# Performance work log

Hardware: AMD Instinct MI355X
Metric: run time of the kernel (lower is better)

## Reference

```python
import jax, jax.numpy as jnp
import numpy as np

DIM = 1024
B = 8192
DT_REF_BASE = 1.0


def _cayley(raw_re, raw_im):
    # A = skew-Hermitian-ish combo per original code
    A = (raw_re - raw_re.T) * 0.5 + 1j * ((raw_im + raw_im.T) * 0.5)
    I = jnp.eye(A.shape[0], dtype=A.dtype)
    return jnp.linalg.solve(I - A, I + A)


def setup_inputs() -> dict:
    key = jax.random.key(0)
    ks = jax.random.split(key, 16)
    d = DIM
    g = d // 2  # n_groups = 2, equal group sizes
    return {
        "h_prev": jax.random.normal(ks[0], (B, d), jnp.float32),
        "x_input": jax.random.normal(ks[1], (B, d), jnp.float32),
        "dt": jax.random.uniform(ks[2], (B,), jnp.float32),
        "u_raw_re": jax.random.normal(ks[3], (d, d), jnp.float32) * 0.01,
        "u_raw_im": jax.random.normal(ks[4], (d, d), jnp.float32) * 0.01,
        "v_raw_re": jax.random.normal(ks[5], (d, d), jnp.float32) * 0.01,
        "v_raw_im": jax.random.normal(ks[6], (d, d), jnp.float32) * 0.01,
        "log_sigma": jnp.zeros((d,), jnp.float32),
        "ld": jax.random.normal(ks[7], (d,), jnp.float32) * 0.5 - 2.0,
        "lf": jnp.concatenate([
            2.0 * jax.random.normal(ks[8], (g,), jnp.float32),
            0.1 * jax.random.normal(ks[9], (g,), jnp.float32),
        ]),
        "dt_scaler": jnp.concatenate([0.1 * jnp.ones((g,), jnp.float32),
                                      10.0 * jnp.ones((g,), jnp.float32)]),
        "src_re": jax.random.normal(ks[10], (d,), jnp.float32) * 0.01,
        "src_im": jax.random.normal(ks[11], (d,), jnp.float32) * 0.01,
        "law_re": jax.random.normal(ks[12], (d,), jnp.float32) * 0.01,
        "law_im": jax.random.normal(ks[13], (d,), jnp.float32) * 0.01,
        "sel_w": jax.random.normal(ks[14], (2 * d, 2 * d), jnp.float32) * 0.01,
        "sel_b": jax.random.normal(ks[15], (2 * d,), jnp.float32) * 0.01,
    }


def reference(h_prev, x_input, dt, u_raw_re, u_raw_im, v_raw_re, v_raw_im,
              log_sigma, ld, lf, dt_scaler, src_re, src_im, law_re, law_im,
              sel_w, sel_b):
    # --- Cayley basis (shared between encode/decode) ---
    U = _cayley(u_raw_re, u_raw_im)                       # [D, D] complex
    V = _cayley(v_raw_re, v_raw_im)
    s = jnp.exp(log_sigma).astype(U.dtype)
    s_inv = jnp.exp(-log_sigma).astype(U.dtype)
    M_inv = (V * s_inv[None, :]) @ U.conj().T             # V @ diag(1/s) @ U^H
    M = (U * s[None, :]) @ V.conj().T                     # U @ diag(s) @ V^H

    encode = lambda x: x.astype(M_inv.dtype) @ M_inv.T
    h_tilde = encode(h_prev)[:, None, :]                  # [B, 1, D]
    x_tilde = encode(x_input)[:, None, :]                 # [B, 1, D]
    x_state = x_tilde[:, 0, :]                            # [B, D]

    # --- selective Lambda ---
    lam_static = (-jnp.exp(ld) + 1j * lf) + (law_re + 1j * law_im)  # [D]
    x_cat = jnp.concatenate([x_state.real, x_state.imag], axis=-1)  # [B, 2D]
    delta = x_cat @ sel_w.T + sel_b                                  # [B, 2D]
    d_re, d_im = jnp.split(delta, 2, axis=-1)
    Lam = lam_static[None, :] + (d_re + 1j * d_im)                   # [B, D]

    # --- transition operators ---
    dt_ref_eff = DT_REF_BASE * dt_scaler                  # [D]
    dt_n = dt[:, None] / dt_ref_eff                       # [B, D]
    Z = Lam * dt_n.astype(Lam.dtype)
    mask = jnp.abs(Z) < 1e-4
    safe_Z = jnp.where(mask, jnp.ones_like(Z), Z)
    phi1 = jnp.where(mask, 1.0 + 0.5 * Z + Z * Z / 6.0,
                     (jnp.exp(Z) - 1.0) / safe_Z)
    op_decay = jnp.exp(Z)                                 # [B, D]
    op_forcing = phi1 * (dt_n * dt_ref_eff).astype(Z.dtype)

    bias = src_re + 1j * src_im                           # [D]
    h_next = h_tilde * op_decay[:, None, :] + (x_tilde + bias) * op_forcing[:, None, :]
    # eval mode / noise term omitted (deterministic reference)
    return h_next @ M.T                                   # [B, 1, D] complex64
```

## Files before the change

### kernel.cpp

```cpp
#include <hip/hip_runtime.h>
#include <hip/hip_bf16.h>

#define Dd 1024
#define Bb 8192

typedef unsigned short u16;
typedef __attribute__((ext_vector_type(8))) short short8;
typedef __attribute__((ext_vector_type(4))) float f32x4;
typedef __attribute__((ext_vector_type(4))) float float4v;

static constexpr size_t DD  = (size_t)Dd * Dd;
static constexpr size_t BD  = (size_t)Bb * Dd;
static constexpr size_t MBy = 1ull << 20;

__device__ __forceinline__ float bf2f(u16 v) {
  union { unsigned u; float f; } c; c.u = ((unsigned)v) << 16; return c.f;
}
__device__ __forceinline__ u16 f2bf(float f) {
  union { float f; unsigned u; } c; c.f = f;
  return (u16)((c.u + 0x7fffu + ((c.u >> 16) & 1u)) >> 16);
}

union U64 { u16 u[4]; unsigned long long v; };

struct ZP { const u16* Ah; const u16* Al; const u16* Bh; const u16* Bl; void* C; void* C2; float alpha; float beta; };
struct GArgs { ZP z[8]; int K, lda, ldb; long ldc; int cstride; };

template<int OUT>
__device__ __forceinline__ void c_store(const ZP& p, long cidx, float acc) {
  float v = acc * p.alpha;
  if constexpr (OUT == 1) {
    ((u16*)p.C)[cidx] = f2bf(v);
  } else if constexpr (OUT == 2) {
    u16 h = f2bf(v);
    ((u16*)p.C)[cidx] = h;
    ((u16*)p.C2)[cidx] = f2bf(v - bf2f(h));
  } else {
    float* C = (float*)p.C;
    if (p.beta != 0.0f) v += p.beta * C[cidx];
    C[cidx] = v;
  }
}

template<int MODE, int OUT>
__global__ __launch_bounds__(256) void gemm_nt(GArgs a) {
  constexpr bool X2 = (MODE != 0);
  constexpr int BK  = X2 ? 32 : 64;
  constexpr int BUFS = 16384;
  __shared__ __align__(16) u16 smem[2 * BUFS];
  const ZP p = a.z[blockIdx.z];
  const int tid  = threadIdx.x;
  const int lane = tid & 63, wv = tid >> 6;

  int bx = blockIdx.x, by = blockIdx.y;
  {
    const int gx = gridDim.x;
    const int nwg = gx * gridDim.y;
    if ((nwg & 7) == 0 && nwg >= 16) {
      const int flat = by * gx + bx;
      const int ch = nwg >> 3;
      const int nf = (flat & 7) * ch + (flat >> 3);
      bx = nf % gx; by = nf / gx;
    }
  }

  const long brow = (long)by * 128, bcol = (long)bx * 128;
  const int wm = (wv & 1) * 64, wn = (wv >> 1) * 64;
  const int srow = wv * 8 + (lane >> 3);
  const int sgc64 = ((lane & 7) ^ (lane >> 3)) * 8;
  const int sgc32 = ((tid & 3) ^ ((tid >> 3) & 3)) * 8;

  f32x4 acc[4][4];
#pragma unroll
  for (int i = 0; i < 4; ++i)
#pragma unroll
    for (int j = 0; j < 4; ++j) { f32x4 zv = {0.f, 0.f, 0.f, 0.f}; acc[i][j] = zv; }

  auto STAGE = [&](int kt, int buf) {
    u16* base = smem + buf * BUFS;
    if constexpr (!X2) {
      u16* As = base;
      u16* Bs = base + 8192;
#pragma unroll
      for (int i = 0; i < 4; ++i) {
        const int rr = i * 32 + srow;
        const int lb = (i * 32 + wv * 8) * 64;
        const u16* ga = p.Ah + (brow + rr) * (long)a.lda + kt + sgc64;
        const u16* gb = p.Bh + (bcol + rr) * (long)a.ldb + kt + sgc64;
        __builtin_amdgcn_global_load_lds((const __attribute__((address_space(1))) void*)ga,
                                         (__attribute__((address_space(3))) void*)(As + lb), 16, 0, 0);
        __builtin_amdgcn_global_load_lds((const __attribute__((address_space(1))) void*)gb,
                                         (__attribute__((address_space(3))) void*)(Bs + lb), 16, 0, 0);
      }
    } else {
#pragma unroll
      for (int pass = 0; pass < 2; ++pass) {
        const int row = pass * 64 + (tid >> 2);
        const int lb = pass * 2048 + tid * 8;
        const u16* ga = p.Ah + (brow + row) * (long)a.lda + kt + sgc32;
        const u16* gb = p.Bh + (bcol + row) * (long)a.ldb + kt + sgc32;
        const u16* ga2 = p.Al + (brow + row) * (long)a.lda + kt + sgc32;
        const u16* gb2 = p.Bl + (bcol + row) * (long)a.ldb + kt + sgc32;
        __builtin_amdgcn_global_load_lds((const __attribute__((address_space(1))) void*)ga,
                                         (__attribute__((address_space(3))) void*)(base + lb), 16, 0, 0);
        __builtin_amdgcn_global_load_lds((const __attribute__((address_space(1))) void*)gb,
                                         (__attribute__((address_space(3))) void*)(base + 4096 + lb), 16, 0, 0);
        __builtin_amdgcn_global_load_lds((const __attribute__((address_space(1))) void*)ga2,
                                         (__attribute__((address_space(3))) void*)(base + 8192 + lb), 16, 0, 0);
        __builtin_amdgcn_global_load_lds((const __attribute__((address_space(1))) void*)gb2,
                                         (__attribute__((address_space(3))) void*)(base + 12288 + lb), 16, 0, 0);
      }
    }
  };

  auto COMPUTE = [&](int buf) {
    u16* base = smem + buf * BUFS;
    if constexpr (!X2) {
      u16* As = base;
      u16* Bs = base + 8192;
#pragma unroll
      for (int kk = 0; kk < 64; kk += 32) {
        const int jf = (kk >> 3) + (lane >> 4);
        const int cs = ((jf ^ (lane & 7)) << 3);
        short8 af[4], bfv[4];
#pragma unroll
        for (int i = 0; i < 4; ++i) {
          af[i]  = *(const short8*)(As + (wm + i * 16 + (lane & 15)) * 64 + cs);
          bfv[i] = *(const short8*)(Bs + (wn + i * 16 + (lane & 15)) * 64 + cs);
        }
#pragma unroll
        for (int i = 0; i < 4; ++i)
#pragma unroll
          for (int j = 0; j < 4; ++j)
            acc[i][j] = __builtin_amdgcn_mfma_f32_16x16x32_bf16(af[i], bfv[j], acc[i][j], 0, 0, 0);
      }
    } else {
      const int jf = lane >> 4;
      const int cs = ((jf ^ ((lane >> 1) & 3)) << 3);
      short8 af[4], bfv[4], al[4], bl[4];
#pragma unroll
      for (int i = 0; i < 4; ++i) {
        const int ra = (wm + i * 16 + (lane & 15)) * 32 + cs;
        const int rb = (wn + i * 16 + (lane & 15)) * 32 + cs;
        af[i]  = *(const short8*)(base + ra);
        bfv[i] = *(const short8*)(base + 4096 + rb);
        al[i]  = *(const short8*)(base + 8192 + ra);
        bl[i]  = *(const short8*)(base + 12288 + rb);
      }
#pragma unroll
      for (int i = 0; i < 4; ++i)
#pragma unroll
        for (int j = 0; j < 4; ++j) {
          acc[i][j] = __builtin_amdgcn_mfma_f32_16x16x32_bf16(af[i], bfv[j], acc[i][j], 0, 0, 0);
          acc[i][j] = __builtin_amdgcn_mfma_f32_16x16x32_bf16(al[i], bfv[j], acc[i][j], 0, 0, 0);
          acc[i][j] = __builtin_amdgcn_mfma_f32_16x16x32_bf16(af[i], bl[j], acc[i][j], 0, 0, 0);
        }
    }
  };

  const int nkt = a.K / BK;
  STAGE(0, 0);
  __syncthreads();
  int cur = 0;
  for (int t = 0; t < nkt - 1; ++t) {
    STAGE((t + 1) * BK, cur ^ 1);
    COMPUTE(cur);
    __syncthreads();
    cur ^= 1;
  }
  COMPUTE(cur);

  const long crow = brow + wm + ((lane >> 4) * 4);
  const long ccol = bcol + wn + (lane & 15);
#pragma unroll
  for (int i = 0; i < 4; ++i)
#pragma unroll
    for (int j = 0; j < 4; ++j)
#pragma unroll
      for (int r = 0; r < 4; ++r) {
        const long cidx = (crow + i * 16 + r) * a.ldc + (ccol + j * 16) * (long)a.cstride;
        c_store<OUT>(p, cidx, acc[i][j][r]);
      }
}

template<int OUT>
__global__ __launch_bounds__(512, 1) void gemm_nt256(GArgs a) {
  constexpr int BUFS = 32768;
  __shared__ __align__(16) u16 smem[2 * BUFS];
  const ZP p = a.z[blockIdx.z];
  const int tid  = threadIdx.x;
  const int lane = tid & 63, wv = tid >> 6;
  const int wr = wv >> 2, wc = wv & 3;

  int bx = blockIdx.x, by = blockIdx.y;
  {
    const int gx = gridDim.x;
    const int nwg = gx * gridDim.y;
    if ((nwg & 7) == 0 && nwg >= 16) {
      const int flat = by * gx + bx;
      const int ch = nwg >> 3;
      const int nf = (flat & 7) * ch + (flat >> 3);
      bx = nf % gx; by = nf / gx;
    }
  }

  const long brow = (long)by * 256, bcol = (long)bx * 256;
  const int sgc = ((tid & 7) ^ ((tid >> 3) & 7)) * 8;

  f32x4 acc[8][4];
#pragma unroll
  for (int i = 0; i < 8; ++i)
#pragma unroll
    for (int j = 0; j < 4; ++j) { f32x4 zv = {0.f, 0.f, 0.f, 0.f}; acc[i][j] = zv; }

  auto STAGE = [&](int kt, int buf) {
    u16* As = smem + buf * BUFS;
    u16* Bs = As + 16384;
#pragma unroll
    for (int i = 0; i < 4; ++i) {
      const int rr = i * 64 + (tid >> 3);
      const int lb = i * 4096 + tid * 8;
      const u16* ga = p.Ah + (brow + rr) * (long)a.lda + kt + sgc;
      const u16* gb = p.Bh + (bcol + rr) * (long)a.ldb + kt + sgc;
      __builtin_amdgcn_global_load_lds((const __attribute__((address_space(1))) void*)ga,
                                       (__attribute__((address_space(3))) void*)(As + lb), 16, 0, 0);
      __builtin_amdgcn_global_load_lds((const __attribute__((address_space(1))) void*)gb,
                                       (__attribute__((address_space(3))) void*)(Bs + lb), 16, 0, 0);
    }
  };

  auto COMPUTE = [&](int buf) {
    u16* As = smem + buf * BUFS;
    u16* Bs = As + 16384;
#pragma unroll
    for (int kk = 0; kk < 64; kk += 32) {
      const int jf = (kk >> 3) + (lane >> 4);
      const int cs = ((jf ^ (lane & 7)) << 3);
      short8 af[8], bfv[4];
#pragma unroll
      for (int i = 0; i < 8; ++i)
        af[i] = *(const short8*)(As + (wr * 128 + i * 16 + (lane & 15)) * 64 + cs);
#pragma unroll
      for (int j = 0; j < 4; ++j)
        bfv[j] = *(const short8*)(Bs + (wc * 64 + j * 16 + (lane & 15)) * 64 + cs);
#pragma unroll
      for (int i = 0; i < 8; ++i)
#pragma unroll
        for (int j = 0; j < 4; ++j)
          acc[i][j] = __builtin_amdgcn_mfma_f32_16x16x32_bf16(af[i], bfv[j], acc[i][j], 0, 0, 0);
    }
  };

  const int nkt = a.K >> 6;
  STAGE(0, 0);
  __syncthreads();
  int cur = 0;
  for (int t = 0; t < nkt - 1; ++t) {
    STAGE((t + 1) * 64, cur ^ 1);
    COMPUTE(cur);
    __syncthreads();
    cur ^= 1;
  }
  COMPUTE(cur);

  const long crow = brow + wr * 128 + ((lane >> 4) * 4);
  const long ccol = bcol + wc * 64 + (lane & 15);
#pragma unroll
  for (int i = 0; i < 8; ++i)
#pragma unroll
    for (int j = 0; j < 4; ++j)
#pragma unroll
      for (int r = 0; r < 4; ++r) {
        const long cidx = (crow + i * 16 + r) * a.ldc + (ccol + j * 16) * (long)a.cstride;
        c_store<OUT>(p, cidx, acc[i][j][r]);
      }
}

#define TLOAD(ldsbuf, srcp) do { \
  _Pragma("unroll") \
  for (int i_ = 0; i_ < 4; ++i_) { \
    int row_ = ty + i_ * 16; \
    float4v v_ = *(const float4v*)((srcp) + (size_t)row_ * Dd + tx * 4); \
    ldsbuf[row_][tx * 4 + 0] = v_[0]; ldsbuf[row_][tx * 4 + 1] = v_[1]; \
    ldsbuf[row_][tx * 4 + 2] = v_[2]; ldsbuf[row_][tx * 4 + 3] = v_[3]; \
  } } while (0)

__global__ void k_buildA(const float* ur, const float* ui, const float* vr, const float* vi,
                         float* Af32, u16* Ahi, u16* Alo, u16* AsumH, u16* AsumL) {
  __shared__ float ldsA[64][65], ldsB[64][65];
  const int y = blockIdx.z;
  const int tx = threadIdx.x & 15, ty = threadIdx.x >> 4;
  const int R0 = blockIdx.y * 64, C0 = blockIdx.x * 64;
  const float* re = y ? vr : ur; const float* im = y ? vi : ui;
  TLOAD(ldsA, re + (size_t)C0 * Dd + R0);
  TLOAD(ldsB, im + (size_t)C0 * Dd + R0);
  __syncthreads();
#pragma unroll
  for (int i = 0; i < 4; ++i) {
    const int r = R0 + ty + i * 16;
    const size_t base = (size_t)r * Dd + C0 + tx * 4;
    float4v vre = *(const float4v*)(re + base);
    float4v vim = *(const float4v*)(im + base);
    float4v oar, oai;
    U64 ph, pl, pih, pil, sh, sl;
#pragma unroll
    for (int j = 0; j < 4; ++j) {
      float are = 0.5f * (vre[j] - ldsA[tx * 4 + j][ty + i * 16]);
      float aim = 0.5f * (vim[j] + ldsB[tx * 4 + j][ty + i * 16]);
      oar[j] = are; oai[j] = aim;
      u16 h = f2bf(are); ph.u[j] = h; pl.u[j] = f2bf(are - bf2f(h));
      h = f2bf(aim); pih.u[j] = h; pil.u[j] = f2bf(aim - bf2f(h));
      float s = are + aim; h = f2bf(s); sh.u[j] = h; sl.u[j] = f2bf(s - bf2f(h));
    }
    const size_t pr = (size_t)y * 2 * DD + base, pi = pr + DD;
    *(float4v*)(Af32 + pr) = oar; *(float4v*)(Af32 + pi) = oai;
    *(unsigned long long*)(Ahi + pr) = ph.v; *(unsigned long long*)(Alo + pr) = pl.v;
    *(unsigned long long*)(Ahi + pi) = pih.v; *(unsigned long long*)(Alo + pi) = pil.v;
    const size_t ps = (size_t)y * DD + base;
    *(unsigned long long*)(AsumH + ps) = sh.v; *(unsigned long long*)(AsumL + ps) = sl.v;
  }
}

__global__ void k_sq(const float* T, float* A2u, float* A2v, u16* A2T, u16* A2Tsum) {
  __shared__ float ldsA[64][65], ldsB[64][65];
  const int y = blockIdx.z;
  const int tx = threadIdx.x & 15, ty = threadIdx.x >> 4;
  const int R0 = blockIdx.y * 64, C0 = blockIdx.x * 64;
  const float* t0p = T + (size_t)y * 3 * DD;
  const float* t2p = t0p + 2 * DD;
  TLOAD(ldsA, t2p + (size_t)C0 * Dd + R0);
  __syncthreads();
  float* A2 = y ? A2v : A2u;
  float xr[4][4], xi[4][4];
#pragma unroll
  for (int i = 0; i < 4; ++i) {
    const size_t base = (size_t)(R0 + ty + i * 16) * Dd + C0 + tx * 4;
    float4v v0 = *(const float4v*)(t0p + base);
    float4v v1 = *(const float4v*)(t0p + DD + base);
    float4v v2 = *(const float4v*)(t2p + base);
    float4v oar, oai;
#pragma unroll
    for (int j = 0; j < 4; ++j) {
      float a2re = -v0[j] - v1[j];
      float a2im = v2[j] - ldsA[tx * 4 + j][ty + i * 16];
      xr[i][j] = a2re; xi[i][j] = a2im;
      oar[j] = a2re; oai[j] = a2im;
    }
    *(float4v*)(A2 + base) = oar;
    *(float4v*)(A2 + DD + base) = oai;
  }
  __syncthreads();
#pragma unroll
  for (int i = 0; i < 4; ++i)
#pragma unroll
    for (int j = 0; j < 4; ++j) {
      ldsA[ty + i * 16][tx * 4 + j] = xr[i][j];
      ldsB[ty + i * 16][tx * 4 + j] = xi[i][j];
    }
  __syncthreads();
#pragma unroll
  for (int i = 0; i < 4; ++i) {
    const int cc = C0 + ty + i * 16;
    const size_t tb = (size_t)cc * Dd + R0 + tx * 4;
    U64 ph, pih, sh;
#pragma unroll
    for (int j = 0; j < 4; ++j) {
      float a2re = ldsA[tx * 4 + j][ty + i * 16];
      float a2im = ldsB[tx * 4 + j][ty + i * 16];
      ph.u[j] = f2bf(a2re); pih.u[j] = f2bf(a2im);
      sh.u[j] = f2bf(a2re + a2im);
    }
    const size_t qr = (size_t)y * 2 * DD + tb;
    *(unsigned long long*)(A2T + qr) = ph.v;
    *(unsigned long long*)(A2T + qr + DD) = pih.v;
    *(unsigned long long*)(A2Tsum + (size_t)y * DD + tb) = sh.v;
  }
}

__global__ void k_x0n(const float* Af32, const float* A2u, const float* A2v, const float* T,
                      float* Xf32, u16* Xhi, u16* XThi, u16* XsumH, u16* XTsumH) {
  __shared__ float ldsA[64][65], ldsB[64][65];
  const int y = blockIdx.z;
  const int tx = threadIdx.x & 15, ty = threadIdx.x >> 4;
  const int R0 = blockIdx.y * 64, C0 = blockIdx.x * 64;
  const float* t0p = T + (size_t)y * 3 * DD;
  const float* A2 = y ? A2v : A2u;
  float xr[4][4], xi[4][4];
#pragma unroll
  for (int i = 0; i < 4; ++i) {
    const int r = R0 + ty + i * 16;
    const size_t base = (size_t)r * Dd + C0 + tx * 4;
    float4v v0 = *(const float4v*)(t0p + base);
    float4v v1 = *(const float4v*)(t0p + DD + base);
    float4v v2 = *(const float4v*)(t0p + 2 * DD + base);
    const size_t pr = (size_t)y * 2 * DD + base, pi = pr + DD;
    float4v ar = *(const float4v*)(Af32 + pr);
    float4v ai = *(const float4v*)(Af32 + pi);
    float4v a2r = *(const float4v*)(A2 + base);
    float4v a2i = *(const float4v*)(A2 + DD + base);
    float4v oxr, oxi;
    U64 ph, pih, sh;
#pragma unroll
    for (int j = 0; j < 4; ++j) {
      const int c = C0 + tx * 4 + j;
      float xre = ar[j] + a2r[j] + (v0[j] - v1[j]) + (r == c ? 1.0f : 0.0f);
      float xim = ai[j] + a2i[j] + (v2[j] - v0[j] - v1[j]);
      xr[i][j] = xre; xi[i][j] = xim;
      oxr[j] = xre; oxi[j] = xim;
      ph.u[j] = f2bf(xre); pih.u[j] = f2bf(xim);
      sh.u[j] = f2bf(xre + xim);
    }
    *(float4v*)(Xf32 + pr) = oxr; *(float4v*)(Xf32 + pi) = oxi;
    *(unsigned long long*)(Xhi + pr) = ph.v; *(unsigned long long*)(Xhi + pi) = pih.v;
    *(unsigned long long*)(XsumH + (size_t)y * DD + base) = sh.v;
  }
  __syncthreads();
#pragma unroll
  for (int i = 0; i < 4; ++i)
#pragma unroll
    for (int j = 0; j < 4; ++j) {
      ldsA[ty + i * 16][tx * 4 + j] = xr[i][j];
      ldsB[ty + i * 16][tx * 4 + j] = xi[i][j];
    }
  __syncthreads();
#pragma unroll
  for (int i = 0; i < 4; ++i) {
    const int cc = C0 + ty + i * 16;
    const size_t tb = (size_t)cc * Dd + R0 + tx * 4;
    U64 ph, pih, sh;
#pragma unroll
    for (int j = 0; j < 4; ++j) {
      float xre = ldsA[tx * 4 + j][ty + i * 16];
      float xim = ldsB[tx * 4 + j][ty + i * 16];
      ph.u[j] = f2bf(xre); pih.u[j] = f2bf(xim);
      sh.u[j] = f2bf(xre + xim);
    }
    const size_t qr = (size_t)y * 2 * DD + tb;
    *(unsigned long long*)(XThi + qr) = ph.v;
    *(unsigned long long*)(XThi + qr + DD) = pih.v;
    *(unsigned long long*)(XTsumH + (size_t)y * DD + tb) = sh.v;
  }
}

__global__ void k_wt(const float* Xf32, const float* T, u16* WThi, u16* WTsumH, float idc) {
  __shared__ float lds[64][65];
  const int y = blockIdx.z;
  const int tx = threadIdx.x & 15, ty = threadIdx.x >> 4;
  const int N0 = blockIdx.y * 64, K0 = blockIdx.x * 64;
  const float* t1p = T + (size_t)y * 3 * DD;
  const float* xrp = Xf32 + (size_t)y * 2 * DD;
  float wre[4][4], wim[4][4];
#pragma unroll
  for (int i = 0; i < 4; ++i)
#pragma unroll
    for (int j = 0; j < 4; ++j) {
      wre[i][j] = ((N0 + ty + i * 16) == (K0 + tx * 4 + j)) ? idc : 0.0f;
      wim[i][j] = 0.0f;
    }
  const float* planes[5] = {t1p, t1p + DD, t1p + 2 * DD, xrp, xrp + DD};
#pragma unroll
  for (int p = 0; p < 5; ++p) {
    TLOAD(lds, planes[p] + (size_t)K0 * Dd + N0);
    __syncthreads();
#pragma unroll
    for (int i = 0; i < 4; ++i)
#pragma unroll
      for (int j = 0; j < 4; ++j) {
        float v = lds[tx * 4 + j][ty + i * 16];
        if (p == 0) { wre[i][j] += v; wim[i][j] -= v; }
        else if (p == 1) { wre[i][j] -= v; wim[i][j] -= v; }
        else if (p == 2) { wim[i][j] += v; }
        else if (p == 3) { wre[i][j] -= v; }
        else { wim[i][j] -= v; }
      }
    __syncthreads();
  }
#pragma unroll
  for (int i = 0; i < 4; ++i) {
    const size_t base = (size_t)(N0 + ty + i * 16) * Dd + K0 + tx * 4;
    U64 ph, pih, sh;
#pragma unroll
    for (int j = 0; j < 4; ++j) {
      ph.u[j] = f2bf(wre[i][j]); pih.u[j] = f2bf(wim[i][j]);
      sh.u[j] = f2bf(wre[i][j] + wim[i][j]);
    }
    const size_t pr = (size_t)y * 2 * DD + base;
    *(unsigned long long*)(WThi + pr) = ph.v;
    *(unsigned long long*)(WThi + pr + DD) = pih.v;
    *(unsigned long long*)(WTsumH + (size_t)y * DD + base) = sh.v;
  }
}

__global__ void k_xn(const float* T, float* Xf32, u16* Xhi, u16* XThi, u16* XsumH, u16* XTsumH,
                     u16* Xlo, u16* XTlo, u16* XTsumL) {
  __shared__ float ldsA[64][65], ldsB[64][65];
  const int y = blockIdx.z;
  const int tx = threadIdx.x & 15, ty = threadIdx.x >> 4;
  const int R0 = blockIdx.y * 64, C0 = blockIdx.x * 64;
  const float* t1p = T + (size_t)y * 3 * DD;
  float xr[4][4], xi[4][4];
#pragma unroll
  for (int i = 0; i < 4; ++i) {
    const size_t base = (size_t)(R0 + ty + i * 16) * Dd + C0 + tx * 4;
    float4v v1 = *(const float4v*)(t1p + base);
    float4v v2 = *(const float4v*)(t1p + DD + base);
    float4v v3 = *(const float4v*)(t1p + 2 * DD + base);
    float4v oxr, oxi;
    U64 ph, pih, sh, plr, pli;
#pragma unroll
    for (int j = 0; j < 4; ++j) {
      float xre = v1[j] - v2[j];
      float xim = v3[j] - v1[j] - v2[j];
      xr[i][j] = xre; xi[i][j] = xim;
      oxr[j] = xre; oxi[j] = xim;
      u16 hr = f2bf(xre), hi_ = f2bf(xim);
      ph.u[j] = hr; pih.u[j] = hi_;
      sh.u[j] = f2bf(xre + xim);
      plr.u[j] = f2bf(xre - bf2f(hr)); pli.u[j] = f2bf(xim - bf2f(hi_));
    }
    const size_t pr = (size_t)y * 2 * DD + base, pi = pr + DD;
    *(float4v*)(Xf32 + pr) = oxr; *(float4v*)(Xf32 + pi) = oxi;
    *(unsigned long long*)(Xhi + pr) = ph.v; *(unsigned long long*)(Xhi + pi) = pih.v;
    *(unsigned long long*)(XsumH + (size_t)y * DD + base) = sh.v;
    if (Xlo) {
      *(unsigned long long*)(Xlo + pr) = plr.v;
      *(unsigned long long*)(Xlo + pi) = pli.v;
    }
  }
  __syncthreads();
#pragma unroll
  for (int i = 0; i < 4; ++i)
#pragma unroll
    for (int j = 0; j < 4; ++j) {
      ldsA[ty + i * 16][tx * 4 + j] = xr[i][j];
      ldsB[ty + i * 16][tx * 4 + j] = xi[i][j];
    }
  __syncthreads();
#pragma unroll
  for (int i = 0; i < 4; ++i) {
    const int cc = C0 + ty + i * 16;
    const size_t tb = (size_t)cc * Dd + R0 + tx * 4;
    U64 ph, pih, sh, plr, pli, sl;
#pragma unroll
    for (int j = 0; j < 4; ++j) {
      float xre = ldsA[tx * 4 + j][ty + i * 16];
      float xim = ldsB[tx * 4 + j][ty + i * 16];
      u16 hr = f2bf(xre), hi_ = f2bf(xim);
      ph.u[j] = hr; pih.u[j] = hi_;
      float s = xre + xim; u16 hs = f2bf(s);
      sh.u[j] = hs;
      plr.u[j] = f2bf(xre - bf2f(hr)); pli.u[j] = f2bf(xim - bf2f(hi_));
      sl.u[j] = f2bf(s - bf2f(hs));
    }
    const size_t qr = (size_t)y * 2 * DD + tb;
    *(unsigned long long*)(XThi + qr) = ph.v;
    *(unsigned long long*)(XThi + qr + DD) = pih.v;
    *(unsigned long long*)(XTsumH + (size_t)y * DD + tb) = sh.v;
    if (Xlo) {
      *(unsigned long long*)(XTlo + qr) = plr.v;
      *(unsigned long long*)(XTlo + qr + DD) = pli.v;
      *(unsigned long long*)(XTsumL + (size_t)y * DD + tb) = sl.v;
    }
  }
}

__global__ void k_finalUV(const float* Xf32, const float* T, const float* logsig,
                          u16* VsHi, u16* VsLo, u16* UHi, u16* ULo, u16* UsHi, u16* VHi,
                          u16* UdifH, u16* UdifL, u16* UssumH, u16* VssumH, u16* VssumL, u16* VdifH) {
  const int y = blockIdx.y;
  const size_t idx = (size_t)blockIdx.x * 256 + threadIdx.x;
  const size_t r = idx >> 10, c = idx & 1023;
  const size_t t0 = (size_t)y * 3 * DD;
  float t1 = T[t0 + idx], t2 = T[t0 + DD + idx], t3 = T[t0 + 2 * DD + idx];
  const size_t pr = (size_t)y * 2 * DD + idx, pi = pr + DD;
  float cre = 2.0f * (Xf32[pr] + (t1 - t2)) - (r == c ? 1.0f : 0.0f);
  float cim = 2.0f * (Xf32[pi] + (t3 - t1 - t2));
  if (y == 0) {
    u16 h = f2bf(cre); UHi[idx] = h; ULo[idx] = f2bf(cre - bf2f(h));
    h = f2bf(cim); UHi[DD + idx] = h; ULo[DD + idx] = f2bf(cim - bf2f(h));
    float d = cre - cim; h = f2bf(d); UdifH[idx] = h; UdifL[idx] = f2bf(d - bf2f(h));
    float s = expf(logsig[c]);
    UsHi[idx] = f2bf(cre * s); UsHi[DD + idx] = f2bf(cim * s);
    UssumH[idx] = f2bf((cre + cim) * s);
  } else {
    VHi[idx] = f2bf(cre); VHi[DD + idx] = f2bf(cim);
    VdifH[idx] = f2bf(cre - cim);
    float si = expf(-logsig[c]);
    float a = cre * si, b = cim * si;
    u16 h = f2bf(a); VsHi[idx] = h; VsLo[idx] = f2bf(a - bf2f(h));
    h = f2bf(b); VsHi[DD + idx] = h; VsLo[DD + idx] = f2bf(b - bf2f(h));
    float ss = (cre + cim) * si; h = f2bf(ss); VssumH[idx] = h; VssumL[idx] = f2bf(ss - bf2f(h));
  }
}

__global__ void k_cmb_M(const float* T, u16* MiRe, u16* MiIm, u16* MiTcH, u16* MiTcL,
                        u16* Mcat) {
  __shared__ float ldsA[64][65], ldsB[64][65];
  const int tx = threadIdx.x & 15, ty = threadIdx.x >> 4;
  const int R0 = blockIdx.y * 64, C0 = blockIdx.x * 64;
#pragma unroll
  for (int i = 0; i < 4; ++i) {
    const size_t base = (size_t)(R0 + ty + i * 16) * Dd + C0 + tx * 4;
    const size_t r = R0 + ty + i * 16;
    float4v g1 = *(const float4v*)(T + base);
    float4v g2 = *(const float4v*)(T + DD + base);
    float4v g3 = *(const float4v*)(T + 2 * DD + base);
    float4v h1 = *(const float4v*)(T + 3 * DD + base);
    float4v h2 = *(const float4v*)(T + 4 * DD + base);
    float4v h3 = *(const float4v*)(T + 5 * DD + base);
    U64 pir, pii, pmr, pmi;
#pragma unroll
    for (int j = 0; j < 4; ++j) {
      float mire = g1[j] + g2[j];
      float miim = g3[j] - g1[j] + g2[j];
      float mre  = h1[j] + h2[j];
      float mim  = h3[j] - h1[j] + h2[j];
      pir.u[j] = f2bf(mire); pii.u[j] = f2bf(miim);
      pmr.u[j] = f2bf(mre);  pmi.u[j] = f2bf(mim);
      ldsA[ty + i * 16][tx * 4 + j] = mire;
      ldsB[ty + i * 16][tx * 4 + j] = miim;
    }
    *(unsigned long long*)(MiRe + base) = pir.v;
    *(unsigned long long*)(MiIm + base) = pii.v;
    const size_t mb = r * 2048 + C0 + tx * 4;
    *(unsigned long long*)(Mcat + mb) = pmr.v;
    *(unsigned long long*)(Mcat + mb + 1024) = pmi.v;
  }
  __syncthreads();
#pragma unroll
  for (int i = 0; i < 4; ++i) {
    const int cc = C0 + ty + i * 16;
    const size_t o = (size_t)cc * 2048 + R0 + tx * 4;
    U64 rh, rl, ih, il;
#pragma unroll
    for (int j = 0; j < 4; ++j) {
      float mire = ldsA[tx * 4 + j][ty + i * 16];
      float miim = ldsB[tx * 4 + j][ty + i * 16];
      u16 h = f2bf(mire); rh.u[j] = h; rl.u[j] = f2bf(mire - bf2f(h));
      h = f2bf(miim); ih.u[j] = h; il.u[j] = f2bf(miim - bf2f(h));
    }
    *(unsigned long long*)(MiTcH + o) = rh.v;
    *(unsigned long long*)(MiTcL + o) = rl.v;
    *(unsigned long long*)(MiTcH + o + 1024) = ih.v;
    *(unsigned long long*)(MiTcL + o + 1024) = il.v;
  }
}

__global__ void k_split4(const float* src, u16* hi, u16* lo) {
  const size_t i4 = (size_t)blockIdx.x * 256 + threadIdx.x;
  float4v v = ((const float4v*)src)[i4];
  U64 oh, ol;
#pragma unroll
  for (int j = 0; j < 4; ++j) {
    u16 h = f2bf(v[j]);
    oh.u[j] = h; ol.u[j] = f2bf(v[j] - bf2f(h));
  }
  ((unsigned long long*)hi)[i4] = oh.v;
  ((unsigned long long*)lo)[i4] = ol.v;
}

__global__ void k_splitB(const float* x, const float* hsrc, u16* xh, u16* xl, u16* hb) {
  const size_t i4 = (size_t)blockIdx.x * 256 + threadIdx.x;
  float4v xv = ((const float4v*)x)[i4];
  float4v hv = ((const float4v*)hsrc)[i4];
  U64 oh, ol, ob;
#pragma unroll
  for (int j = 0; j < 4; ++j) {
    u16 h = f2bf(xv[j]);
    oh.u[j] = h;
    ol.u[j] = f2bf(xv[j] - bf2f(h));
    ob.u[j] = f2bf(hv[j]);
  }
  ((unsigned long long*)xh)[i4] = oh.v;
  ((unsigned long long*)xl)[i4] = ol.v;
  ((unsigned long long*)hb)[i4] = ob.v;
}

__global__ void k_pointwise(const u16* HtCat, const u16* XtCat,
                            const float* delta, const float* dt, const float* ld, const float* lf,
                            const float* dts, const float* sre, const float* sim,
                            const float* lwre, const float* lwim, const float* selb,
                            u16* Hncat, float imSign) {
  const int b = blockIdx.x;
  const int c0 = threadIdx.x * 4;
  const size_t ro = (size_t)b * 2048 + c0;
  const float dtv = dt[b];
  float4v dre4 = *(const float4v*)(delta + ro);
  float4v dim4 = *(const float4v*)(delta + ro + 1024);
  float4v sbR = *(const float4v*)(selb + c0);
  float4v sbI = *(const float4v*)(selb + 1024 + c0);
  float4v ld4 = *(const float4v*)(ld + c0);
  float4v lf4 = *(const float4v*)(lf + c0);
  float4v dts4 = *(const float4v*)(dts + c0);
  float4v sre4 = *(const float4v*)(sre + c0);
  float4v sim4 = *(const float4v*)(sim + c0);
  float4v lwr4 = *(const float4v*)(lwre + c0);
  float4v lwi4 = *(const float4v*)(lwim + c0);
  U64 htR, htI, xtR, xtI;
  htR.v = *(const unsigned long long*)(HtCat + ro);
  htI.v = *(const unsigned long long*)(HtCat + ro + 1024);
  xtR.v = *(const unsigned long long*)(XtCat + ro);
  xtI.v = *(const unsigned long long*)(XtCat + ro + 1024);
  U64 oR, oI;
#pragma unroll
  for (int j = 0; j < 4; ++j) {
    float lamre = -expf(ld4[j]) + lwr4[j] + dre4[j] + sbR[j];
    float lamim = lf4[j] + lwi4[j] + dim4[j] + sbI[j];
    float dtn = dtv / dts4[j];
    float zre = lamre * dtn, zim = lamim * dtn;
    float r2 = zre * zre + zim * zim;
    float er = expf(zre); float sn, cs; __sincosf(zim, &sn, &cs);
    float dcre = er * cs, dcim = er * sn;
    float p1re, p1im;
    if (r2 < 1e-8f) {
      p1re = 1.0f + 0.5f * zre + (zre * zre - zim * zim) * (1.0f / 6.0f);
      p1im = 0.5f * zim + (zre * zim) * (1.0f / 3.0f);
    } else {
      float inv = 1.0f / r2;
      float nre = dcre - 1.0f, nim = dcim;
      p1re = (nre * zre + nim * zim) * inv;
      p1im = (nim * zre - nre * zim) * inv;
    }
    float fre = p1re * dtv, fim = p1im * dtv;
    float hre = bf2f(htR.u[j]), him = bf2f(htI.u[j]);
    float xre = bf2f(xtR.u[j]) + sre4[j], xim = bf2f(xtI.u[j]) + sim4[j];
    float ore = hre * dcre - him * dcim + xre * fre - xim * fim;
    float oim = hre * dcim + him * dcre + xre * fim + xim * fre;
    oR.u[j] = f2bf(ore); oI.u[j] = f2bf(imSign * oim);
  }
  *(unsigned long long*)(Hncat + ro) = oR.v;
  *(unsigned long long*)(Hncat + ro + 1024) = oI.v;
}

__global__ void k_fill(float* p, size_t n, float v) {
  const size_t idx = (size_t)blockIdx.x * 256 + threadIdx.x;
  if (idx < n) p[idx] = v;
}

static void launch_gemm(int mode, int out, int M, int N, int K, int lda, int ldb,
                        long ldc, int cstride, int nz, const ZP* z, hipStream_t s) {
  GArgs a; a.K = K; a.lda = lda; a.ldb = ldb; a.ldc = ldc; a.cstride = cstride;
  for (int i = 0; i < 8; ++i) a.z[i] = z[i < nz ? i : 0];
  dim3 g(N / 128, M / 128, nz), blk(256);
  if (mode == 1 && out == 0)      gemm_nt<1, 0><<<g, blk, 0, s>>>(a);
  else if (mode == 1 && out == 2) gemm_nt<1, 2><<<g, blk, 0, s>>>(a);
  else if (out == 1)              gemm_nt<0, 1><<<g, blk, 0, s>>>(a);
  else                            gemm_nt<0, 0><<<g, blk, 0, s>>>(a);
}

static void launch_gemm256(int out, int M, int N, int K, int lda, int ldb,
                           long ldc, int cstride, int nz, const ZP* z, hipStream_t s) {
  GArgs a; a.K = K; a.lda = lda; a.ldb = ldb; a.ldc = ldc; a.cstride = cstride;
  for (int i = 0; i < 8; ++i) a.z[i] = z[i < nz ? i : 0];
  dim3 g(N / 256, M / 256, nz), blk(512);
  if (out == 1) gemm_nt256<1><<<g, blk, 0, s>>>(a);
  else          gemm_nt256<0><<<g, blk, 0, s>>>(a);
}

extern "C" void kernel_launch(void* const* d_in, const int* in_sizes, int n_in,
                              void* d_out, int out_size, void* d_ws, size_t ws_size,
                              hipStream_t stream) {
  const float* h_prev  = (const float*)d_in[0];
  const float* x_input = (const float*)d_in[1];
  const float* dt      = (const float*)d_in[2];
  const float* ur      = (const float*)d_in[3];
  const float* ui      = (const float*)d_in[4];
  const float* vr      = (const float*)d_in[5];
  const float* vi      = (const float*)d_in[6];
  const float* logsig  = (const float*)d_in[7];
  const float* ld      = (const float*)d_in[8];
  const float* lf      = (const float*)d_in[9];
  const float* dts     = (const float*)d_in[10];
  const float* sre     = (const float*)d_in[11];
  const float* sim     = (const float*)d_in[12];
  const float* lwre    = (const float*)d_in[13];
  const float* lwim    = (const float*)d_in[14];
  const float* sel_w   = (const float*)d_in[15];
  const float* sel_b   = (const float*)d_in[16];
  float* out = (float*)d_out;
  char* ws = (char*)d_ws;

  const bool realOnly = ((size_t)out_size == BD);
  const bool interleaved = ((size_t)out_size == 2 * BD);
  if ((!realOnly && !interleaved) || ws_size < 224 * MBy) {
    k_fill<<<dim3(((size_t)out_size + 255) / 256), dim3(256), 0, stream>>>(out, (size_t)out_size, 1e9f);
    return;
  }

  u16* MiRe_b = (u16*)(ws + 0 * MBy);
  u16* MiIm_b = (u16*)(ws + 2 * MBy);
  u16* Mcat   = (u16*)(ws + 4 * MBy);
  u16* G_hi   = (u16*)(ws + 8 * MBy);
  u16* G_lo   = (u16*)(ws + 12 * MBy);
  char* AR = ws + 16 * MBy;
  float* Af32   = (float*)(AR + 0);
  u16* Ahi      = (u16*)(AR + 16 * MBy);
  u16* Alo      = (u16*)(AR + 24 * MBy);
  u16* AsumH    = (u16*)(AR + 32 * MBy);
  u16* AsumL    = (u16*)(AR + 36 * MBy);
  float* Xf32   = (float*)(AR + 40 * MBy);
  u16* Xhi      = (u16*)(AR + 56 * MBy);
  u16* Xlo      = (u16*)(AR + 64 * MBy);
  u16* XThi     = (u16*)(AR + 72 * MBy);
  u16* XTlo     = (u16*)(AR + 80 * MBy);
  u16* XsumH    = (u16*)(AR + 88 * MBy);
  u16* XTsumH   = (u16*)(AR + 92 * MBy);
  u16* XTsumL   = (u16*)(AR + 96 * MBy);
  u16* WThi     = (u16*)(AR + 100 * MBy);
  u16* WTsumH   = (u16*)(AR + 108 * MBy);
  float* T      = (float*)(AR + 112 * MBy);
  u16* VsHi     = (u16*)(AR + 136 * MBy);
  u16* VsLo     = (u16*)(AR + 140 * MBy);
  u16* UHi      = (u16*)(AR + 144 * MBy);
  u16* ULo      = (u16*)(AR + 148 * MBy);
  u16* UsHi     = (u16*)(AR + 152 * MBy);
  u16* VHi      = (u16*)(AR + 156 * MBy);
  u16* UdifH    = (u16*)(AR + 160 * MBy);
  u16* UdifL    = (u16*)(AR + 162 * MBy);
  u16* UssumH   = (u16*)(AR + 164 * MBy);
  u16* VssumH   = (u16*)(AR + 166 * MBy);
  u16* VssumL   = (u16*)(AR + 168 * MBy);
  u16* VdifH    = (u16*)(AR + 170 * MBy);
  u16* MiTcH    = (u16*)(AR + 172 * MBy);
  u16* MiTcL    = (u16*)(AR + 176 * MBy);
  u16* W_hi     = (u16*)(AR + 180 * MBy);
  u16* W_lo     = (u16*)(AR + 188 * MBy);
  float* A2u    = (float*)(AR + 64 * MBy);
  float* A2v    = (float*)(AR + 80 * MBy);
  u16* A2T      = (u16*)(AR + 100 * MBy);
  u16* A2Tsum   = (u16*)(AR + 108 * MBy);
  u16* Hb     = (u16*)(AR + 0);
  u16* XbHi   = (u16*)(AR + 16 * MBy);
  u16* XbLo   = (u16*)(AR + 32 * MBy);
  u16* HtCat  = (u16*)(AR + 48 * MBy);
  u16* XtCat  = (u16*)(AR + 80 * MBy);
  float* delta= (float*)(AR + 112 * MBy);
  u16* Hncat  = (u16*)(AR + 176 * MBy);

  dim3 b256(256);
  const dim3 tdd(16, 16, 2);

  k_buildA<<<tdd, b256, 0, stream>>>(ur, ui, vr, vi, Af32, Ahi, Alo, AsumH, AsumL);

  {
    ZP z[6];
    for (int y = 0; y < 2; ++y) {
      const u16* are = Ahi + (size_t)y * 2 * DD; const u16* aim = are + DD;
      float* t = T + (size_t)y * 3 * DD;
      z[y*3+0] = {are, nullptr, are, nullptr, t,          nullptr, 1.f, 0.f};
      z[y*3+1] = {aim, nullptr, aim, nullptr, t + DD,     nullptr, 1.f, 0.f};
      z[y*3+2] = {are, nullptr, aim, nullptr, t + 2*DD,   nullptr, 1.f, 0.f};
    }
    launch_gemm(0, 0, 1024, 1024, 1024, 1024, 1024, 1024, 1, 6, z, stream);
  }
  k_sq<<<tdd, b256, 0, stream>>>(T, A2u, A2v, A2T, A2Tsum);
  {
    ZP z[6];
    for (int y = 0; y < 2; ++y) {
      const u16* are = Ahi + (size_t)y*2*DD; const u16* aim = are + DD;
      const u16* a2r = A2T + (size_t)y*2*DD; const u16* a2i = a2r + DD;
      float* t = T + (size_t)y*3*DD;
      z[y*3+0] = {are, nullptr, a2r, nullptr, t,        nullptr, 1.f, 0.f};
      z[y*3+1] = {aim, nullptr, a2i, nullptr, t + DD,   nullptr, 1.f, 0.f};
      z[y*3+2] = {AsumH + (size_t)y*DD, nullptr, A2Tsum + (size_t)y*DD, nullptr, t + 2*DD, nullptr, 1.f, 0.f};
    }
    launch_gemm(0, 0, 1024, 1024, 1024, 1024, 1024, 1024, 1, 6, z, stream);
  }
  k_x0n<<<tdd, b256, 0, stream>>>(Af32, A2u, A2v, T, Xf32, Xhi, XThi, XsumH, XTsumH);

  {
    ZP z[6];
    for (int y = 0; y < 2; ++y) {
      const u16* are = Ahi + (size_t)y*2*DD; const u16* aim = are + DD;
      const u16* xtr = XThi + (size_t)y*2*DD; const u16* xti = xtr + DD;
      float* t = T + (size_t)y*3*DD;
      z[y*3+0] = {are, nullptr, xtr, nullptr, t,        nullptr, 1.f, 0.f};
      z[y*3+1] = {aim, nullptr, xti, nullptr, t + DD,   nullptr, 1.f, 0.f};
      z[y*3+2] = {AsumH + (size_t)y*DD, nullptr, XTsumH + (size_t)y*DD, nullptr, t + 2*DD, nullptr, 1.f, 0.f};
    }
    launch_gemm(0, 0, 1024, 1024, 1024, 1024, 1024, 1024, 1, 6, z, stream);
  }
  k_wt<<<tdd, b256, 0, stream>>>(Xf32, T, WThi, WTsumH, 2.0f);
  {
    ZP z[6];
    for (int y = 0; y < 2; ++y) {
      const u16* xre = Xhi + (size_t)y*2*DD; const u16* xim = xre + DD;
      const u16* wtr = WThi + (size_t)y*2*DD; const u16* wti = wtr + DD;
      float* t = T + (size_t)y*3*DD;
      z[y*3+0] = {xre, nullptr, wtr, nullptr, t,        nullptr, 1.f, 0.f};
      z[y*3+1] = {xim, nullptr, wti, nullptr, t + DD,   nullptr, 1.f, 0.f};
      z[y*3+2] = {XsumH + (size_t)y*DD, nullptr, WTsumH + (size_t)y*DD, nullptr, t + 2*DD, nullptr, 1.f, 0.f};
    }
    launch_gemm(0, 0, 1024, 1024, 1024, 1024, 1024, 1024, 1, 6, z, stream);
  }
  k_xn<<<tdd, b256, 0, stream>>>(T, Xf32, Xhi, XThi, XsumH, XTsumH, Xlo, XTlo, XTsumL);

  {
    ZP z[6];
    for (int y = 0; y < 2; ++y) {
      const u16* areh = Ahi + (size_t)y*2*DD; const u16* aimh = areh + DD;
      const u16* arel = Alo + (size_t)y*2*DD; const u16* aiml = arel + DD;
      const u16* xtrh = XThi + (size_t)y*2*DD; const u16* xtih = xtrh + DD;
      const u16* xtrl = XTlo + (size_t)y*2*DD; const u16* xtil = xtrl + DD;
      float* t = T + (size_t)y*3*DD;
      z[y*3+0] = {areh, arel, xtrh, xtrl, t,        nullptr, 1.f, 0.f};
      z[y*3+1] = {aimh, aiml, xtih, xtil, t + DD,   nullptr, 1.f, 0.f};
      z[y*3+2] = {AsumH + (size_t)y*DD, AsumL + (size_t)y*DD,
                  XTsumH + (size_t)y*DD, XTsumL + (size_t)y*DD, t + 2*DD, nullptr, 1.f, 0.f};
    }
    launch_gemm(1, 0, 1024, 1024, 1024, 1024, 1024, 1024, 1, 6, z, stream);
  }
  k_wt<<<tdd, b256, 0, stream>>>(Xf32, T, WThi, WTsumH, 1.0f);
  {
    ZP z[6];
    for (int y = 0; y < 2; ++y) {
      const u16* xre = Xhi + (size_t)y*2*DD; const u16* xim = xre + DD;
      const u16* rtr = WThi + (size_t)y*2*DD; const u16* rti = rtr + DD;
      float* t = T + (size_t)y*3*DD;
      z[y*3+0] = {xre, nullptr, rtr, nullptr, t,        nullptr, 1.f, 0.f};
      z[y*3+1] = {xim, nullptr, rti, nullptr, t + DD,   nullptr, 1.f, 0.f};
      z[y*3+2] = {XsumH + (size_t)y*DD, nullptr, WTsumH + (size_t)y*DD, nullptr, t + 2*DD, nullptr, 1.f, 0.f};
    }
    launch_gemm(0, 0, 1024, 1024, 1024, 1024, 1024, 1024, 1, 6, z, stream);
  }
  k_finalUV<<<dim3(4096, 2), b256, 0, stream>>>(Xf32, T, logsig, VsHi, VsLo, UHi, ULo, UsHi, VHi,
                                                UdifH, UdifL, UssumH, VssumH, VssumL, VdifH);

  {
    ZP z[3] = {
      {VsHi,      VsLo,      UHi,      ULo,      T,        nullptr, 1.f, 0.f},
      {VsHi + DD, VsLo + DD, UHi + DD, ULo + DD, T + DD,   nullptr, 1.f, 0.f},
      {VssumH,    VssumL,    UdifH,    UdifL,    T + 2*DD, nullptr, 1.f, 0.f}};
    launch_gemm(1, 0, 1024, 1024, 1024, 1024, 1024, 1024, 1, 3, z, stream);
  }
  {
    ZP z[3] = {
      {UsHi,      nullptr, VHi,      nullptr, T + 3*DD, nullptr, 1.f, 0.f},
      {UsHi + DD, nullptr, VHi + DD, nullptr, T + 4*DD, nullptr, 1.f, 0.f},
      {UssumH,    nullptr, VdifH,    nullptr, T + 5*DD, nullptr, 1.f, 0.f}};
    launch_gemm(0, 0, 1024, 1024, 1024, 1024, 1024, 1024, 1, 3, z, stream);
  }
  k_cmb_M<<<dim3(16, 16), b256, 0, stream>>>(T, MiRe_b, MiIm_b, MiTcH, MiTcL, Mcat);

  k_split4<<<dim3(4096), b256, 0, stream>>>(sel_w, W_hi, W_lo);
  {
    ZP z1[1] = {{W_hi, W_lo, MiTcH, MiTcL, G_hi, G_lo, 1.f, 0.f}};
    launch_gemm(1, 2, 2048, 1024, 2048, 2048, 2048, 1024, 1, 1, z1, stream);
  }

  k_splitB<<<dim3(8192), b256, 0, stream>>>(x_input, h_prev, XbHi, XbLo, Hb);
  {
    ZP z[2] = {
      {Hb,   nullptr, MiRe_b, nullptr, HtCat, nullptr, 1.f, 0.f},
      {XbHi, nullptr, MiRe_b, nullptr, XtCat, nullptr, 1.f, 0.f}};
    launch_gemm256(1, 8192, 2048, 1024, 1024, 1024, 2048, 1, 2, z, stream);
  }
  {
    ZP z[2] = {
      {XbHi, XbLo, G_hi,                     G_lo,                     delta,        nullptr, 1.f, 0.f},
      {XbHi, XbLo, G_hi + 1024 * (size_t)Dd, G_lo + 1024 * (size_t)Dd, delta + 1024, nullptr, 1.f, 0.f}};
    launch_gemm(1, 0, 8192, 512, 1024, 1024, 1024, 2048, 1, 2, z, stream);
  }
  {
    ZP z[2] = {
      {XbHi, nullptr, G_hi + 512 * (size_t)Dd,  nullptr, delta + 512,  nullptr, 1.f, 0.f},
      {XbHi, nullptr, G_hi + 1536 * (size_t)Dd, nullptr, delta + 1536, nullptr, 1.f, 0.f}};
    launch_gemm(0, 0, 8192, 512, 1024, 1024, 1024, 2048, 1, 2, z, stream);
  }

  if (realOnly) {
    k_pointwise<<<dim3(8192), b256, 0, stream>>>(HtCat, XtCat, delta, dt, ld, lf, dts,
                                                 sre, sim, lwre, lwim, sel_b, Hncat, -1.0f);
    ZP z1[1] = {{Hncat, nullptr, Mcat, nullptr, out, nullptr, 1.f, 0.f}};
    launch_gemm(0, 0, 8192, 1024, 2048, 2048, 2048, 1024, 1, 1, z1, stream);
  } else {
    k_pointwise<<<dim3(8192), b256, 0, stream>>>(HtCat, XtCat, delta, dt, ld, lf, dts,
                                                 sre, sim, lwre, lwim, sel_b, Hncat, -1.0f);
    {
      ZP z1[1] = {{Hncat, nullptr, Mcat, nullptr, out, nullptr, 1.f, 0.f}};
      launch_gemm(0, 0, 8192, 1024, 2048, 2048, 2048, 2048, 2, 1, z1, stream);
    }
    {
      ZP z1[1] = {{Hncat, nullptr, Mcat + 1024, nullptr, out + 1, nullptr, 1.f, 0.f}};
      launch_gemm(0, 0, 8192, 1024, 1024, 2048, 2048, 2048, 2, 1, z1, stream);
    }
    {
      ZP z1[1] = {{Hncat + 1024, nullptr, Mcat, nullptr, out + 1, nullptr, -1.f, 1.f}};
      launch_gemm(0, 0, 8192, 1024, 1024, 2048, 2048, 2048, 2, 1, z1, stream);
    }
  }
}
```

Before: 616.0 us.

## Retile GEMMs: narrow split-precision tiles, switch plain GEMMs to 256 tiles

Adds a BN template parameter to the 128-row gemm_nt kernel and launches it with 64-wide column tiles. For the split-precision delta GEMM this doubles the number of workgroups and shrinks the shared-memory footprint. The plain bf16 GEMMs (the narrow delta half and the final projection(s) onto M) move to the 256x256-tile, 512-thread kernel, for more operand reuse per block. The risk is that the large tiles give only about 128 workgroups for these shapes, which may leave many CUs idle.

```diff
diff --git a/kernel.cpp b/kernel.cpp
--- a/kernel.cpp
+++ b/kernel.cpp
@@ -42,11 +42,15 @@
   }
 }
 
-template<int MODE, int OUT>
+template<int MODE, int OUT, int BN>
 __global__ __launch_bounds__(256) void gemm_nt(GArgs a) {
   constexpr bool X2 = (MODE != 0);
   constexpr int BK  = X2 ? 32 : 64;
-  constexpr int BUFS = 16384;
+  constexpr int NJ  = BN / 32;
+  constexpr int BUFS = 8192 + BN * 64;
+  constexpr int BHOFF = 4096;
+  constexpr int ALOFF = 4096 + BN * 32;
+  constexpr int BLOFF = 8192 + BN * 32;
   __shared__ __align__(16) u16 smem[2 * BUFS];
   const ZP p = a.z[blockIdx.z];
   const int tid  = threadIdx.x;
@@ -64,17 +68,17 @@
     }
   }
 
-  const long brow = (long)by * 128, bcol = (long)bx * 128;
-  const int wm = (wv & 1) * 64, wn = (wv >> 1) * 64;
+  const long brow = (long)by * 128, bcol = (long)bx * BN;
+  const int wm = (wv & 1) * 64, wn = (wv >> 1) * (BN / 2);
   const int srow = wv * 8 + (lane >> 3);
   const int sgc64 = ((lane & 7) ^ (lane >> 3)) * 8;
   const int sgc32 = ((tid & 3) ^ ((tid >> 3) & 3)) * 8;
 
-  f32x4 acc[4][4];
+  f32x4 acc[4][NJ];
 #pragma unroll
   for (int i = 0; i < 4; ++i)
 #pragma unroll
-    for (int j = 0; j < 4; ++j) { f32x4 zv = {0.f, 0.f, 0.f, 0.f}; acc[i][j] = zv; }
+    for (int j = 0; j < NJ; ++j) { f32x4 zv = {0.f, 0.f, 0.f, 0.f}; acc[i][j] = zv; }
 
   auto STAGE = [&](int kt, int buf) {
     u16* base = smem + buf * BUFS;
@@ -86,9 +90,14 @@
         const int rr = i * 32 + srow;
         const int lb = (i * 32 + wv * 8) * 64;
         const u16* ga = p.Ah + (brow + rr) * (long)a.lda + kt + sgc64;
-        const u16* gb = p.Bh + (bcol + rr) * (long)a.ldb + kt + sgc64;
         __builtin_amdgcn_global_load_lds((const __attribute__((address_space(1))) void*)ga,
                                          (__attribute__((address_space(3))) void*)(As + lb), 16, 0, 0);
+      }
+#pragma unroll
+      for (int i = 0; i < BN / 32; ++i) {
+        const int rr = i * 32 + srow;
+        const int lb = (i * 32 + wv * 8) * 64;
+        const u16* gb = p.Bh + (bcol + rr) * (long)a.ldb + kt + sgc64;
         __builtin_amdgcn_global_load_lds((const __attribute__((address_space(1))) void*)gb,
                                          (__attribute__((address_space(3))) void*)(Bs + lb), 16, 0, 0);
       }
@@ -98,17 +107,22 @@
         const int row = pass * 64 + (tid >> 2);
         const int lb = pass * 2048 + tid * 8;
         const u16* ga = p.Ah + (brow + row) * (long)a.lda + kt + sgc32;
-        const u16* gb = p.Bh + (bcol + row) * (long)a.ldb + kt + sgc32;
         const u16* ga2 = p.Al + (brow + row) * (long)a.lda + kt + sgc32;
-        const u16* gb2 = p.Bl + (bcol + row) * (long)a.ldb + kt + sgc32;
         __builtin_amdgcn_global_load_lds((const __attribute__((address_space(1))) void*)ga,
                                          (__attribute__((address_space(3))) void*)(base + lb), 16, 0, 0);
+        __builtin_amdgcn_global_load_lds((const __attribute__((address_space(1))) void*)ga2,
+                                         (__attribute__((address_space(3))) void*)(base + ALOFF + lb), 16, 0, 0);
+      }
+#pragma unroll
+      for (int pass = 0; pass < BN / 64; ++pass) {
+        const int row = pass * 64 + (tid >> 2);
+        const int lb = pass * 2048 + tid * 8;
+        const u16* gb = p.Bh + (bcol + row) * (long)a.ldb + kt + sgc32;
+        const u16* gb2 = p.Bl + (bcol + row) * (long)a.ldb + kt + sgc32;
         __builtin_amdgcn_global_load_lds((const __attribute__((address_space(1))) void*)gb,
-                                         (__attribute__((address_space(3))) void*)(base + 4096 + lb), 16, 0, 0);
-        __builtin_amdgcn_global_load_lds((const __attribute__((address_space(1))) void*)ga2,
-                                         (__attribute__((address_space(3))) void*)(base + 8192 + lb), 16, 0, 0);
+                                         (__attribute__((address_space(3))) void*)(base + BHOFF + lb), 16, 0, 0);
         __builtin_amdgcn_global_load_lds((const __attribute__((address_space(1))) void*)gb2,
-                                         (__attribute__((address_space(3))) void*)(base + 12288 + lb), 16, 0, 0);
+                                         (__attribute__((address_space(3))) void*)(base + BLOFF + lb), 16, 0, 0);
       }
     }
   };
@@ -122,35 +136,39 @@
       for (int kk = 0; kk < 64; kk += 32) {
         const int jf = (kk >> 3) + (lane >> 4);
         const int cs = ((jf ^ (lane & 7)) << 3);
-        short8 af[4], bfv[4];
-#pragma unroll
-        for (int i = 0; i < 4; ++i) {
-          af[i]  = *(const short8*)(As + (wm + i * 16 + (lane & 15)) * 64 + cs);
-          bfv[i] = *(const short8*)(Bs + (wn + i * 16 + (lane & 15)) * 64 + cs);
-        }
+        short8 af[4], bfv[NJ];
 #pragma unroll
         for (int i = 0; i < 4; ++i)
-#pragma unroll
-          for (int j = 0; j < 4; ++j)
+          af[i] = *(const short8*)(As + (wm + i * 16 + (lane & 15)) * 64 + cs);
+#pragma unroll
+        for (int j = 0; j < NJ; ++j)
+          bfv[j] = *(const short8*)(Bs + (wn + j * 16 + (lane & 15)) * 64 + cs);
+#pragma unroll
+        for (int i = 0; i < 4; ++i)
+#pragma unroll
+          for (int j = 0; j < NJ; ++j)
             acc[i][j] = __builtin_amdgcn_mfma_f32_16x16x32_bf16(af[i], bfv[j], acc[i][j], 0, 0, 0);
       }
     } else {
       const int jf = lane >> 4;
       const int cs = ((jf ^ ((lane >> 1) & 3)) << 3);
-      short8 af[4], bfv[4], al[4], bl[4];
+      short8 af[4], al[4], bfv[NJ], bl[NJ];
 #pragma unroll
       for (int i = 0; i < 4; ++i) {
         const int ra = (wm + i * 16 + (lane & 15)) * 32 + cs;
-        const int rb = (wn + i * 16 + (lane & 15)) * 32 + cs;
-        af[i]  = *(const short8*)(base + ra);
-        bfv[i] = *(const short8*)(base + 4096 + rb);
-        al[i]  = *(const short8*)(base + 8192 + ra);
-        bl[i]  = *(const short8*)(base + 12288 + rb);
+        af[i] = *(const short8*)(base + ra);
+        al[i] = *(const short8*)(base + ALOFF + ra);
       }
 #pragma unroll
+      for (int j = 0; j < NJ; ++j) {
+        const int rb = (wn + j * 16 + (lane & 15)) * 32 + cs;
+        bfv[j] = *(const short8*)(base + BHOFF + rb);
+        bl[j]  = *(const short8*)(base + BLOFF + rb);
+      }
+#pragma unroll
       for (int i = 0; i < 4; ++i)
 #pragma unroll
-        for (int j = 0; j < 4; ++j) {
+        for (int j = 0; j < NJ; ++j) {
           acc[i][j] = __builtin_amdgcn_mfma_f32_16x16x32_bf16(af[i], bfv[j], acc[i][j], 0, 0, 0);
           acc[i][j] = __builtin_amdgcn_mfma_f32_16x16x32_bf16(al[i], bfv[j], acc[i][j], 0, 0, 0);
           acc[i][j] = __builtin_amdgcn_mfma_f32_16x16x32_bf16(af[i], bl[j], acc[i][j], 0, 0, 0);
@@ -175,7 +193,7 @@
 #pragma unroll
   for (int i = 0; i < 4; ++i)
 #pragma unroll
-    for (int j = 0; j < 4; ++j)
+    for (int j = 0; j < NJ; ++j)
 #pragma unroll
       for (int r = 0; r < 4; ++r) {
         const long cidx = (crow + i * 16 + r) * a.ldc + (ccol + j * 16) * (long)a.cstride;
@@ -741,11 +759,10 @@
                         long ldc, int cstride, int nz, const ZP* z, hipStream_t s) {
   GArgs a; a.K = K; a.lda = lda; a.ldb = ldb; a.ldc = ldc; a.cstride = cstride;
   for (int i = 0; i < 8; ++i) a.z[i] = z[i < nz ? i : 0];
-  dim3 g(N / 128, M / 128, nz), blk(256);
-  if (mode == 1 && out == 0)      gemm_nt<1, 0><<<g, blk, 0, s>>>(a);
-  else if (mode == 1 && out == 2) gemm_nt<1, 2><<<g, blk, 0, s>>>(a);
-  else if (out == 1)              gemm_nt<0, 1><<<g, blk, 0, s>>>(a);
-  else                            gemm_nt<0, 0><<<g, blk, 0, s>>>(a);
+  dim3 g(N / 64, M / 128, nz), blk(256);
+  if (mode == 1 && out == 0)      gemm_nt<1, 0, 64><<<g, blk, 0, s>>>(a);
+  else if (mode == 1 && out == 2) gemm_nt<1, 2, 64><<<g, blk, 0, s>>>(a);
+  else                            gemm_nt<0, 0, 64><<<g, blk, 0, s>>>(a);
 }
 
 static void launch_gemm256(int out, int M, int N, int K, int lda, int ldb,
@@ -965,28 +982,28 @@
     ZP z[2] = {
       {XbHi, nullptr, G_hi + 512 * (size_t)Dd,  nullptr, delta + 512,  nullptr, 1.f, 0.f},
       {XbHi, nullptr, G_hi + 1536 * (size_t)Dd, nullptr, delta + 1536, nullptr, 1.f, 0.f}};
-    launch_gemm(0, 0, 8192, 512, 1024, 1024, 1024, 2048, 1, 2, z, stream);
+    launch_gemm256(0, 8192, 512, 1024, 1024, 1024, 2048, 1, 2, z, stream);
   }
 
   if (realOnly) {
     k_pointwise<<<dim3(8192), b256, 0, stream>>>(HtCat, XtCat, delta, dt, ld, lf, dts,
                                                  sre, sim, lwre, lwim, sel_b, Hncat, -1.0f);
     ZP z1[1] = {{Hncat, nullptr, Mcat, nullptr, out, nullptr, 1.f, 0.f}};
-    launch_gemm(0, 0, 8192, 1024, 2048, 2048, 2048, 1024, 1, 1, z1, stream);
+    launch_gemm256(0, 8192, 1024, 2048, 2048, 2048, 1024, 1, 1, z1, stream);
   } else {
     k_pointwise<<<dim3(8192), b256, 0, stream>>>(HtCat, XtCat, delta, dt, ld, lf, dts,
                                                  sre, sim, lwre, lwim, sel_b, Hncat, -1.0f);
     {
       ZP z1[1] = {{Hncat, nullptr, Mcat, nullptr, out, nullptr, 1.f, 0.f}};
-      launch_gemm(0, 0, 8192, 1024, 2048, 2048, 2048, 2048, 2, 1, z1, stream);
+      launch_gemm256(0, 8192, 1024, 2048, 2048, 2048, 2048, 2, 1, z1, stream);
     }
     {
       ZP z1[1] = {{Hncat, nullptr, Mcat + 1024, nullptr, out + 1, nullptr, 1.f, 0.f}};
-      launch_gemm(0, 0, 8192, 1024, 1024, 2048, 2048, 2048, 2, 1, z1, stream);
+      launch_gemm256(0, 8192, 1024, 1024, 2048, 2048, 2048, 2, 1, z1, stream);
     }
     {
       ZP z1[1] = {{Hncat + 1024, nullptr, Mcat, nullptr, out + 1, nullptr, -1.f, 1.f}};
-      launch_gemm(0, 0, 8192, 1024, 1024, 2048, 2048, 2048, 2, 1, z1, stream);
-    }
-  }
-}
+      launch_gemm256(0, 8192, 1024, 1024, 2048, 2048, 2048, 2, 1, z1, stream);
+    }
+  }
+}
```

New measurement: 637.8 us. 3.5% more time.
